# Optimization experiments

Measured on AMD Instinct MI355X. Metric: run time of the kernel, lower is better.

## Reference

```python
import jax, jax.numpy as jnp
import numpy as np

N_LIG, M_POC = 16384, 32768
E_LIG, E_POC, K_CROSS = 163840, 327680, 8
H = 64
L = 4

silu = jax.nn.silu


def _lin(k, fan_in, fan_out):
    k1, k2 = jax.random.split(k)
    s = 1.0 / np.sqrt(fan_in)
    W = jax.random.uniform(k1, (fan_in, fan_out), jnp.float32, -s, s)
    b = jax.random.uniform(k2, (fan_out,), jnp.float32, -s, s)
    return W, b


def setup_inputs() -> dict:
    key = jax.random.key(0)
    ks = jax.random.split(key, 32)
    inp = {
        'lig_x': jax.random.normal(ks[0], (N_LIG, 3), jnp.float32),
        'lig_h': jax.random.normal(ks[1], (N_LIG, 17), jnp.float32),
        'poc_x': jax.random.normal(ks[2], (M_POC, 3), jnp.float32),
        'poc_h': jax.random.normal(ks[3], (M_POC, 29), jnp.float32),
        'lig_edge_index': jax.random.randint(ks[4], (2, E_LIG), 0, N_LIG, jnp.int32),
        'lig_edge_attr': jax.random.normal(ks[5], (E_LIG, 6), jnp.float32),
        'poc_edge_index': jax.random.randint(ks[6], (2, E_POC), 0, M_POC, jnp.int32),
        'poc_edge_attr': jax.random.normal(ks[7], (E_POC, 16), jnp.float32),
        'cross_edge_index': jnp.stack([
            jax.random.randint(ks[8], (N_LIG * K_CROSS,), 0, M_POC, jnp.int32),
            jax.random.randint(ks[9], (N_LIG * K_CROSS,), 0, N_LIG, jnp.int32)]),
        'cross_edge_attr': jax.random.normal(ks[10], (N_LIG * K_CROSS, 16), jnp.float32),
        't': jax.random.uniform(ks[11], (1,), jnp.float32),
    }
    # embeddings
    inp['lig_emb_W'], inp['lig_emb_b'] = _lin(ks[12], 18, H)
    inp['poc_emb_W'], inp['poc_emb_b'] = _lin(ks[13], 29, H)
    inp['lig_ee_W'], inp['lig_ee_b'] = _lin(ks[14], 6, H)
    inp['poc_ee_W'], inp['poc_ee_b'] = _lin(ks[15], 16, H)
    inp['cross_ee_W'], inp['cross_ee_b'] = _lin(ks[16], 16, H)
    # per-layer params stacked along leading L axis
    def stack(kk, fan_in, fan_out):
        Ws, bs = zip(*[_lin(k, fan_in, fan_out) for k in jax.random.split(kk, L)])
        return jnp.stack(Ws), jnp.stack(bs)
    inp['phi_e_W1'], inp['phi_e_b1'] = stack(ks[17], 2 * H + 1 + H, H)
    inp['phi_e_W2'], inp['phi_e_b2'] = stack(ks[18], H, H)
    inp['phi_x_W1'], inp['phi_x_b1'] = stack(ks[19], H, H)
    inp['phi_x_W2'], inp['phi_x_b2'] = stack(ks[20], H, 1)
    inp['phi_h_W1'], inp['phi_h_b1'] = stack(ks[21], 2 * H, H)
    inp['phi_h_W2'], inp['phi_h_b2'] = stack(ks[22], H, H)
    inp['out_W1'], inp['out_b1'] = _lin(ks[23], H, H)
    inp['out_W2'], inp['out_b2'] = _lin(ks[24], H, 1)
    return inp


def _forward(lig_x, lig_h, poc_x, poc_h, lig_edge_attr, poc_edge_attr,
             cross_edge_attr, t,
             lig_emb_W, lig_emb_b, poc_emb_W, poc_emb_b,
             lig_ee_W, lig_ee_b, poc_ee_W, poc_ee_b, cross_ee_W, cross_ee_b,
             phi_e_W1, phi_e_b1, phi_e_W2, phi_e_b2,
             phi_x_W1, phi_x_b1, phi_x_W2, phi_x_b2,
             phi_h_W1, phi_h_b1, phi_h_W2, phi_h_b2,
             out_W1, out_b1, out_W2, out_b2,
             lig_edge_index, poc_edge_index, cross_edge_index):
    n_lig = lig_h.shape[0]
    n_tot = n_lig + poc_h.shape[0]
    t_feat = jnp.broadcast_to(t.reshape(1, 1), (n_lig, 1))
    h_lig = jnp.concatenate([lig_h, t_feat], -1) @ lig_emb_W + lig_emb_b
    h_poc = poc_h @ poc_emb_W + poc_emb_b
    h = jnp.concatenate([h_lig, h_poc], 0)          # [N, H]
    x = jnp.concatenate([lig_x, poc_x], 0)          # [N, 3]
    src = jnp.concatenate([lig_edge_index[0], poc_edge_index[0] + n_lig,
                           cross_edge_index[0] + n_lig])
    dst = jnp.concatenate([lig_edge_index[1], poc_edge_index[1] + n_lig,
                           cross_edge_index[1]])
    eattr = jnp.concatenate([
        lig_edge_attr @ lig_ee_W + lig_ee_b,
        poc_edge_attr @ poc_ee_W + poc_ee_b,
        cross_edge_attr @ cross_ee_W + cross_ee_b], 0)  # [E, H]
    # True = pocket => coords not updated
    update_mask = jnp.concatenate([
        jnp.ones((n_lig, 1), h.dtype), jnp.zeros((n_tot - n_lig, 1), h.dtype)], 0)
    for i in range(phi_e_W1.shape[0]):
        diff = x[src] - x[dst]                                    # [E, 3]
        dist = jnp.sum(diff * diff, -1, keepdims=True) / 100.0    # [E, 1]
        e_in = jnp.concatenate([h[src], h[dst], dist, eattr], -1) # [E, 2H+1+H]
        m = silu(silu(e_in @ phi_e_W1[i] + phi_e_b1[i]) @ phi_e_W2[i] + phi_e_b2[i])
        cw = jnp.tanh(silu(m @ phi_x_W1[i] + phi_x_b1[i]) @ phi_x_W2[i] + phi_x_b2[i])
        coord_agg = jax.ops.segment_sum(diff * cw, dst, num_segments=n_tot) * update_mask
        msg_agg = jax.ops.segment_sum(m, dst, num_segments=n_tot)
        h = h + silu(jnp.concatenate([h, msg_agg], -1) @ phi_h_W1[i] + phi_h_b1[i]) @ phi_h_W2[i] + phi_h_b2[i]
        x = x + coord_agg
    disp = x[:n_lig] - lig_x
    scale = silu(h[:n_lig] @ out_W1 + out_b1) @ out_W2 + out_b2
    return scale * disp


def reference(lig_x, lig_h, poc_x, poc_h, lig_edge_attr, poc_edge_attr,
              cross_edge_attr, t,
              lig_emb_W, lig_emb_b, poc_emb_W, poc_emb_b,
              lig_ee_W, lig_ee_b, poc_ee_W, poc_ee_b, cross_ee_W, cross_ee_b,
              phi_e_W1, phi_e_b1, phi_e_W2, phi_e_b2,
              phi_x_W1, phi_x_b1, phi_x_W2, phi_x_b2,
              phi_h_W1, phi_h_b1, phi_h_W2, phi_h_b2,
              out_W1, out_b1, out_W2, out_b2,
              lig_edge_index, poc_edge_index, cross_edge_index):
    return _forward(lig_x, lig_h, poc_x, poc_h, lig_edge_attr, poc_edge_attr,
                    cross_edge_attr, t,
                    lig_emb_W, lig_emb_b, poc_emb_W, poc_emb_b,
                    lig_ee_W, lig_ee_b, poc_ee_W, poc_ee_b, cross_ee_W, cross_ee_b,
                    phi_e_W1, phi_e_b1, phi_e_W2, phi_e_b2,
                    phi_x_W1, phi_x_b1, phi_x_W2, phi_x_b2,
                    phi_h_W1, phi_h_b1, phi_h_W2, phi_h_b2,
                    out_W1, out_b1, out_W2, out_b2,
                    lig_edge_index, poc_edge_index, cross_edge_index)
```

## Files before the change

kernel.cpp:

```cpp
#include <hip/hip_runtime.h>

#define N_LIG 16384
#define M_POC 32768
#define N_TOT (N_LIG + M_POC)
#define E_LIG 163840
#define E_POC 327680
#define E_CROSS (N_LIG * 8)
#define E_TOT (E_LIG + E_POC + E_CROSS)
#define TE 16

typedef __bf16 bf16_t;
typedef bf16_t bf16x8 __attribute__((ext_vector_type(8)));
typedef bf16_t bf16x4 __attribute__((ext_vector_type(4)));
typedef bf16_t bf16x2 __attribute__((ext_vector_type(2)));
typedef float f32x4 __attribute__((ext_vector_type(4)));

#define S2 72
#define WAVE_BYTES (1792 + 2304 + 256)

__device__ __forceinline__ float silu_f(float v) { return v / (1.0f + __expf(-v)); }

__device__ __forceinline__ float tanh_f(float v) {
    float a = fabsf(v);
    float t = __expf(-2.0f * a);
    float r = (1.0f - t) / (1.0f + t);
    return copysignf(r, v);
}

__device__ __forceinline__ void atomic_add_f32(float* p, float v) {
    __hip_atomic_fetch_add(p, v, __ATOMIC_RELAXED, __HIP_MEMORY_SCOPE_AGENT);
}

__device__ __forceinline__ void lds_fence() {
    asm volatile("s_waitcnt lgkmcnt(0)" ::: "memory");
}


__global__ void k_build_edges(const int* __restrict__ lig_ei, const int* __restrict__ poc_ei,
                              const int* __restrict__ cross_ei,
                              int* __restrict__ srcA, int* __restrict__ dstA,
                              int* __restrict__ cnt) {
    int e = blockIdx.x * blockDim.x + threadIdx.x;
    if (e < N_TOT) cnt[e] = 0;
    if (e >= E_TOT) return;
    int s, d;
    if (e < E_LIG) {
        s = lig_ei[e];
        d = lig_ei[E_LIG + e];
    } else if (e < E_LIG + E_POC) {
        int i = e - E_LIG;
        s = poc_ei[i] + N_LIG;
        d = poc_ei[E_POC + i] + N_LIG;
    } else {
        int i = e - E_LIG - E_POC;
        s = cross_ei[i] + N_LIG;
        d = cross_ei[E_CROSS + i];
    }
    srcA[e] = s;
    dstA[e] = d;
}

__global__ void k_hist(const int* __restrict__ dstA, int* __restrict__ cnt) {
    int e = blockIdx.x * blockDim.x + threadIdx.x;
    if (e < E_TOT) atomicAdd(&cnt[dstA[e]], 1);
}

__global__ __launch_bounds__(1024) void k_scan(const int* __restrict__ cnt,
                                               int* __restrict__ rowptr,
                                               int* __restrict__ cursor) {
    __shared__ int sums[1024];
    int tid = threadIdx.x;
    int local[48];
    int s = 0;
    for (int i = 0; i < 48; ++i) { local[i] = s; s += cnt[tid * 48 + i]; }
    sums[tid] = s;
    __syncthreads();
    for (int off = 1; off < 1024; off <<= 1) {
        int v = (tid >= off) ? sums[tid - off] : 0;
        __syncthreads();
        sums[tid] += v;
        __syncthreads();
    }
    int base = (tid == 0) ? 0 : sums[tid - 1];
    for (int i = 0; i < 48; ++i) {
        int v = base + local[i];
        int idx = tid * 48 + i;
        rowptr[idx] = v;
        cursor[idx] = v;
    }
    if (tid == 1023) rowptr[N_TOT] = sums[1023];
}

__global__ void k_scatter(const int* __restrict__ dstA, int* __restrict__ cursor,
                          int* __restrict__ sortedPos) {
    int e = blockIdx.x * blockDim.x + threadIdx.x;
    if (e < E_TOT) sortedPos[e] = atomicAdd(&cursor[dstA[e]], 1);
}

#define PK_G1   (12 * 5 * 4 * 64)
#define PK_G23  (4 * 4 * 4 * 64)
#define PK_WP   (4 * 48 * 256)
#define PK_BEFF (12 * 64)
#define PK_TOT  (PK_G1 + PK_G23 + PK_WP + PK_BEFF)

__global__ void k_pack_all(const float* __restrict__ phi_e_W1, const float* __restrict__ phi_e_b1,
                           const float* __restrict__ lig_ee_W, const float* __restrict__ lig_ee_b,
                           const float* __restrict__ poc_ee_W, const float* __restrict__ poc_ee_b,
                           const float* __restrict__ cross_ee_W, const float* __restrict__ cross_ee_b,
                           const float* __restrict__ phi_e_W2, const float* __restrict__ phi_x_W1,
                           const float* __restrict__ phi_h_W1, const float* __restrict__ phi_h_W2,
                           bf16_t* __restrict__ Bg1, bf16_t* __restrict__ Bg23,
                           float* __restrict__ Wp, float* __restrict__ beff) {
    int tid = blockIdx.x * blockDim.x + threadIdx.x;
    if (tid < PK_G1) {
        int lt = tid / 1280;
        int rem = tid - lt * 1280;
        int c = rem >> 8;
        int nt = (rem >> 6) & 3;
        int lane = rem & 63;
        int l = lt / 3, t = lt % 3;
        const float* W1l = phi_e_W1 + l * 193 * 64;
        const float* We; int K;
        if (t == 0) { We = lig_ee_W; K = 6; }
        else if (t == 1) { We = poc_ee_W; K = 16; }
        else { We = cross_ee_W; K = 16; }
        int col = nt * 16 + (lane & 15);
        int k0 = c * 32 + (lane >> 4) * 8;
        #pragma unroll
        for (int j = 0; j < 8; ++j) {
            int row = k0 + j;
            float v = 0.0f;
            if (row < 128) v = W1l[row * 64 + col];
            else if (row < 144) {
                int kk = row - 128;
                if (kk < K) {
                    float a = 0.0f;
                    for (int q = 0; q < 64; ++q) a = fmaf(We[kk * 64 + q], W1l[(129 + q) * 64 + col], a);
                    v = a;
                }
            } else if (row == 144) {
                v = W1l[128 * 64 + col];
            }
            Bg1[(size_t)tid * 8 + j] = (bf16_t)v;
        }
    } else if (tid < PK_G1 + PK_G23) {
        int u = tid - PK_G1;
        int lane = u & 63;
        int nt = (u >> 6) & 3;
        int c = (u >> 8) & 3;
        int l = u >> 10;
        const float* W = (c < 2) ? (phi_e_W2 + l * 4096) : (phi_x_W1 + l * 4096);
        int kb = (c & 1) * 32;
        int col = nt * 16 + (lane & 15);
        int k0 = kb + (lane >> 4) * 8;
        #pragma unroll
        for (int j = 0; j < 8; ++j)
            Bg23[(size_t)u * 8 + j] = (bf16_t)W[(k0 + j) * 64 + col];
    } else if (tid < PK_G1 + PK_G23 + PK_WP) {
        int idx = tid - PK_G1 - PK_G23;
        int l = idx / (48 * 256);
        int rem = idx - l * (48 * 256);
        int c = rem / 256;
        int q = rem - c * 256;
        int j = q >> 2;
        int kk = q & 3;
        const float* W; int Ksrc; int k4;
        if (c < 32) { W = phi_h_W1 + l * 128 * 64; Ksrc = 128; k4 = c; }
        else        { W = phi_h_W2 + l * 64 * 64;  Ksrc = 64;  k4 = c - 32; }
        int k = k4 * 4 + kk;
        Wp[idx] = (k < Ksrc) ? W[k * 64 + j] : 0.0f;
    } else if (tid < PK_TOT) {
        int u = tid - PK_G1 - PK_G23 - PK_WP;
        int j = u & 63;
        int lt = u >> 6;
        int l = lt / 3, t = lt % 3;
        const float* W1l = phi_e_W1 + l * 193 * 64;
        const float* Be = (t == 0) ? lig_ee_b : ((t == 1) ? poc_ee_b : cross_ee_b);
        float v = phi_e_b1[l * 64 + j];
        for (int q = 0; q < 64; ++q) v = fmaf(Be[q], W1l[(129 + q) * 64 + j], v);
        beff[u] = v;
    }
}

__global__ void k_embed(const float* __restrict__ lig_x, const float* __restrict__ lig_h,
                        const float* __restrict__ poc_x, const float* __restrict__ poc_h,
                        const float* __restrict__ t,
                        const float* __restrict__ ligW, const float* __restrict__ ligB,
                        const float* __restrict__ pocW, const float* __restrict__ pocB,
                        float* __restrict__ h, bf16_t* __restrict__ hB, float* __restrict__ x4) {
    int gid = blockIdx.x * blockDim.x + threadIdx.x;
    int n = gid >> 6;
    int lane = gid & 63;
    if (n >= N_TOT) return;
    float a;
    if (n < N_LIG) {
        a = ligB[lane];
        #pragma unroll
        for (int k = 0; k < 17; ++k) a = fmaf(lig_h[n * 17 + k], ligW[k * 64 + lane], a);
        a = fmaf(t[0], ligW[17 * 64 + lane], a);
        if (lane < 4) x4[n * 4 + lane] = (lane < 3) ? lig_x[n * 3 + lane] : 0.0f;
    } else {
        int p = n - N_LIG;
        a = pocB[lane];
        #pragma unroll
        for (int k = 0; k < 29; ++k) a = fmaf(poc_h[p * 29 + k], pocW[k * 64 + lane], a);
        if (lane < 4) x4[n * 4 + lane] = (lane < 3) ? poc_x[p * 3 + lane] : 0.0f;
    }
    h[n * 64 + lane] = a;
    hB[n * 64 + lane] = (bf16_t)a;
}

__global__ __launch_bounds__(256, 6) void k_edge_mfma(
    const bf16_t* __restrict__ hB, const float* __restrict__ x4,
    const int* __restrict__ srcA, const int* __restrict__ dstA,
    const int* __restrict__ sortedPos,
    const float* __restrict__ lig_attr, const float* __restrict__ poc_attr,
    const float* __restrict__ cross_attr,
    const bf16_t* __restrict__ Bg1L,
    const float* __restrict__ beffL,
    const bf16_t* __restrict__ Bg23L,
    const float* __restrict__ b2, const float* __restrict__ bx1,
    const float* __restrict__ Wx2, const float* __restrict__ bx2,
    bf16_t* __restrict__ mBuf, float* __restrict__ coord_agg) {
    __shared__ __align__(16) char lds[4 * WAVE_BYTES];
    const int lane = threadIdx.x & 63;
    const int wave = threadIdx.x >> 6;
    bf16_t* exL = (bf16_t*)(lds + wave * WAVE_BYTES);
    bf16_t* mA  = (bf16_t*)(lds + wave * WAVE_BYTES + 1792);
    float*  dfL = (float*)(lds + wave * WAVE_BYTES + 1792 + 2304);
    const int base = (blockIdx.x * 4 + wave) * TE;

    int tt; const float* attrBase; int astride;
    if (base < E_LIG) { tt = 0; attrBase = lig_attr + (size_t)base * 6; astride = 6; }
    else if (base < E_LIG + E_POC) { tt = 1; attrBase = poc_attr + (size_t)(base - E_LIG) * 16; astride = 16; }
    else { tt = 2; attrBase = cross_attr + (size_t)(base - E_LIG - E_POC) * 16; astride = 16; }

    const int e16 = base + (lane & 15);
    const int sv = srcA[e16];
    const int dv = dstA[e16];
    const int sp = sortedPos[e16];

    const int mcol = lane & 15;
    const int kgrp = lane >> 4;
    const int mrow0 = kgrp * 4;

    bf16x8 af0 = *(const bf16x8*)(hB + (size_t)sv * 64 + kgrp * 8);
    bf16x8 af1 = *(const bf16x8*)(hB + (size_t)sv * 64 + 32 + kgrp * 8);
    bf16x8 af2 = *(const bf16x8*)(hB + (size_t)dv * 64 + kgrp * 8);
    bf16x8 af3 = *(const bf16x8*)(hB + (size_t)dv * 64 + 32 + kgrp * 8);

    {
        bf16x8 z = {(bf16_t)0.f, (bf16_t)0.f, (bf16_t)0.f, (bf16_t)0.f,
                    (bf16_t)0.f, (bf16_t)0.f, (bf16_t)0.f, (bf16_t)0.f};
        *(bf16x8*)(exL + (lane >> 2) * 56 + (lane & 3) * 8) = z;
    }
    lds_fence();
    if (lane < 16) {
        float4 xs = *(const float4*)(x4 + (size_t)sv * 4);
        float4 xd = *(const float4*)(x4 + (size_t)dv * 4);
        float d0 = xs.x - xd.x;
        float d1 = xs.y - xd.y;
        float d2 = xs.z - xd.z;
        float dist = (d0 * d0 + d1 * d1 + d2 * d2) * 0.01f;
        exL[lane * 56 + 16] = (bf16_t)dist;
        *(float4*)(dfL + lane * 4) = (float4){d0, d1, d2, dist};
        const float* attr = attrBase + lane * astride;
        if (tt == 0) {
            float2 a0 = *(const float2*)(attr);
            float2 a1 = *(const float2*)(attr + 2);
            float2 a2 = *(const float2*)(attr + 4);
            bf16x8 w0 = {(bf16_t)a0.x, (bf16_t)a0.y, (bf16_t)a1.x, (bf16_t)a1.y,
                         (bf16_t)a2.x, (bf16_t)a2.y, (bf16_t)0.f, (bf16_t)0.f};
            *(bf16x8*)(exL + lane * 56) = w0;
        } else {
            float4 a0 = *(const float4*)(attr);
            float4 a1 = *(const float4*)(attr + 4);
            float4 a2 = *(const float4*)(attr + 8);
            float4 a3 = *(const float4*)(attr + 12);
            bf16x8 w0 = {(bf16_t)a0.x, (bf16_t)a0.y, (bf16_t)a0.z, (bf16_t)a0.w,
                         (bf16_t)a1.x, (bf16_t)a1.y, (bf16_t)a1.z, (bf16_t)a1.w};
            bf16x8 w1 = {(bf16_t)a2.x, (bf16_t)a2.y, (bf16_t)a2.z, (bf16_t)a2.w,
                         (bf16_t)a3.x, (bf16_t)a3.y, (bf16_t)a3.z, (bf16_t)a3.w};
            *(bf16x8*)(exL + lane * 56) = w0;
            *(bf16x8*)(exL + lane * 56 + 8) = w1;
        }
    }
    lds_fence();

    const bf16_t* Bg1 = Bg1L + (size_t)tt * 5 * 4 * 512;
    const float* beff = beffL + tt * 64;
    f32x4 acc1[4];
    #pragma unroll
    for (int nt = 0; nt < 4; ++nt) {
        float bv = beff[nt * 16 + mcol];
        acc1[nt] = (f32x4){bv, bv, bv, bv};
    }
    bf16x8 af4 = *(const bf16x8*)(exL + mcol * 56 + kgrp * 8);
    bf16x8 afs[5] = {af0, af1, af2, af3, af4};
    #pragma unroll
    for (int c = 0; c < 5; ++c) {
        #pragma unroll
        for (int nt = 0; nt < 4; ++nt) {
            bf16x8 bfr = *(const bf16x8*)(Bg1 + ((size_t)(c * 4 + nt) * 64 + lane) * 8);
            acc1[nt] = __builtin_amdgcn_mfma_f32_16x16x32_bf16(afs[c], bfr, acc1[nt], 0, 0, 0);
        }
    }
    #pragma unroll
    for (int nt = 0; nt < 4; ++nt)
        #pragma unroll
        for (int g = 0; g < 4; ++g)
            mA[(mrow0 + g) * S2 + nt * 16 + mcol] = (bf16_t)silu_f(acc1[nt][g]);
    lds_fence();

    f32x4 acc2[4];
    #pragma unroll
    for (int nt = 0; nt < 4; ++nt) {
        float bv = b2[nt * 16 + mcol];
        acc2[nt] = (f32x4){bv, bv, bv, bv};
    }
    const bf16_t* aBase2 = mA + mcol * S2 + kgrp * 8;
    #pragma unroll
    for (int c = 0; c < 2; ++c) {
        bf16x8 af = *(const bf16x8*)(aBase2 + c * 32);
        #pragma unroll
        for (int nt = 0; nt < 4; ++nt) {
            bf16x8 bfr = *(const bf16x8*)(Bg23L + ((size_t)(c * 4 + nt) * 64 + lane) * 8);
            acc2[nt] = __builtin_amdgcn_mfma_f32_16x16x32_bf16(af, bfr, acc2[nt], 0, 0, 0);
        }
    }
    lds_fence();
    #pragma unroll
    for (int nt = 0; nt < 4; ++nt)
        #pragma unroll
        for (int g = 0; g < 4; ++g)
            mA[(mrow0 + g) * S2 + nt * 16 + mcol] = (bf16_t)silu_f(acc2[nt][g]);
    lds_fence();

    #pragma unroll
    for (int p = 0; p < 2; ++p) {
        const int r = p * 8 + (lane >> 3);
        const int c8 = (lane & 7) * 8;
        bf16x8 mrow = *(const bf16x8*)(mA + r * S2 + c8);
        const int pos = __shfl(sp, r, 64);
        *(bf16x8*)(mBuf + (size_t)pos * 64 + c8) = mrow;
    }

    f32x4 acc3[4];
    #pragma unroll
    for (int nt = 0; nt < 4; ++nt) {
        float bv = bx1[nt * 16 + mcol];
        acc3[nt] = (f32x4){bv, bv, bv, bv};
    }
    const bf16_t* Bg3 = Bg23L + (size_t)2 * 4 * 512;
    #pragma unroll
    for (int c = 0; c < 2; ++c) {
        bf16x8 af = *(const bf16x8*)(aBase2 + c * 32);
        #pragma unroll
        for (int nt = 0; nt < 4; ++nt) {
            bf16x8 bfr = *(const bf16x8*)(Bg3 + ((size_t)(c * 4 + nt) * 64 + lane) * 8);
            acc3[nt] = __builtin_amdgcn_mfma_f32_16x16x32_bf16(af, bfr, acc3[nt], 0, 0, 0);
        }
    }

    const float bx2v = bx2[0];
    float s[4] = {0.f, 0.f, 0.f, 0.f};
    #pragma unroll
    for (int nt = 0; nt < 4; ++nt) {
        float w = Wx2[nt * 16 + mcol];
        #pragma unroll
        for (int g = 0; g < 4; ++g) s[g] = fmaf(silu_f(acc3[nt][g]), w, s[g]);
    }
    #pragma unroll
    for (int g = 0; g < 4; ++g) {
        float p = s[g];
        #pragma unroll
        for (int off = 1; off < 16; off <<= 1) p += __shfl_xor(p, off, 64);
        const float cw = tanh_f(p + bx2v);
        const int d = __shfl(dv, mrow0 + g, 64);
        if (d < N_LIG && mcol < 3)
            atomic_add_f32(&coord_agg[d * 3 + mcol], dfL[(mrow0 + g) * 4 + mcol] * cw);
    }
}

__global__ __launch_bounds__(256) void k_node(
    float* __restrict__ h, bf16_t* __restrict__ hB, float* __restrict__ x4,
    const bf16_t* __restrict__ mBuf, const int* __restrict__ rowptr,
    float* __restrict__ coord,
    const float* __restrict__ Wh1p, const float* __restrict__ bh1,
    const float* __restrict__ Wh2p, const float* __restrict__ bh2) {
    __shared__ __align__(16) float lds[4][TE * 128];
    const int lane = threadIdx.x & 63;
    const int wave = threadIdx.x >> 6;
    float* inL = lds[wave];
    const int base = (blockIdx.x * 4 + wave) * TE;

    #pragma unroll
    for (int i = 0; i < 4; ++i) {
        int fidx = i * 256 + lane * 4;
        float4 v = *(const float4*)(h + (size_t)base * 64 + fidx);
        *(float4*)(inL + (fidx >> 6) * 128 + (fidx & 63)) = v;
    }

    const int n16 = base + (lane & 15);
    const int rp0 = rowptr[n16];
    const int rp1 = rowptr[n16 + 1];
    const int sub = lane >> 4;
    const int f4 = (lane & 15) * 4;
    for (int r = 0; r < TE; ++r) {
        const int s0 = __shfl(rp0, r, 64);
        const int s1 = __shfl(rp1, r, 64);
        float a0 = 0.f, a1 = 0.f, a2 = 0.f, a3 = 0.f;
        for (int i = s0 + sub; i < s1; i += 4) {
            bf16x4 v = *(const bf16x4*)(mBuf + (size_t)i * 64 + f4);
            a0 += (float)v[0]; a1 += (float)v[1]; a2 += (float)v[2]; a3 += (float)v[3];
        }
        a0 += __shfl_xor(a0, 16, 64); a1 += __shfl_xor(a1, 16, 64);
        a2 += __shfl_xor(a2, 16, 64); a3 += __shfl_xor(a3, 16, 64);
        a0 += __shfl_xor(a0, 32, 64); a1 += __shfl_xor(a1, 32, 64);
        a2 += __shfl_xor(a2, 32, 64); a3 += __shfl_xor(a3, 32, 64);
        if (lane < 16)
            *(float4*)(inL + r * 128 + 64 + f4) = (float4){a0, a1, a2, a3};
    }
    __syncthreads();

    float acc[TE];
    #pragma unroll
    for (int r = 0; r < TE; ++r) acc[r] = bh1[lane];
    for (int c = 0; c < 32; ++c) {
        const float4 w = *(const float4*)(Wh1p + (c * 64 + lane) * 4);
        #pragma unroll
        for (int r = 0; r < TE; ++r) {
            const float4 v = *(const float4*)(inL + r * 128 + c * 4);
            acc[r] = fmaf(v.x, w.x, fmaf(v.y, w.y, fmaf(v.z, w.z, fmaf(v.w, w.w, acc[r]))));
        }
    }
    __syncthreads();
    #pragma unroll
    for (int r = 0; r < TE; ++r) inL[r * 64 + lane] = silu_f(acc[r]);
    __syncthreads();

    float acc2[TE];
    #pragma unroll
    for (int r = 0; r < TE; ++r) acc2[r] = bh2[lane];
    for (int c = 0; c < 16; ++c) {
        const float4 w = *(const float4*)(Wh2p + (c * 64 + lane) * 4);
        #pragma unroll
        for (int r = 0; r < TE; ++r) {
            const float4 v = *(const float4*)(inL + r * 64 + c * 4);
            acc2[r] = fmaf(v.x, w.x, fmaf(v.y, w.y, fmaf(v.z, w.z, fmaf(v.w, w.w, acc2[r]))));
        }
    }
    for (int r = 0; r < TE; ++r) {
        const int n = base + r;
        float hv = h[n * 64 + lane] + acc2[r];
        h[n * 64 + lane] = hv;
        hB[n * 64 + lane] = (bf16_t)hv;
        if (lane < 3) {
            if (n < N_LIG) x4[n * 4 + lane] += coord[n * 3 + lane];
            coord[n * 3 + lane] = 0.0f;
        }
    }
}

__global__ void k_out(const float* __restrict__ h, const float* __restrict__ x4,
                      const float* __restrict__ lig_x,
                      const float* __restrict__ oW1, const float* __restrict__ ob1,
                      const float* __restrict__ oW2, const float* __restrict__ ob2,
                      float* __restrict__ out) {
    int gid = blockIdx.x * blockDim.x + threadIdx.x;
    int n = gid >> 6;
    int lane = gid & 63;
    if (n >= N_LIG) return;
    float hv = h[n * 64 + lane];
    float a = ob1[lane];
    #pragma unroll
    for (int k = 0; k < 64; ++k) a = fmaf(__shfl(hv, k, 64), oW1[k * 64 + lane], a);
    float p = silu_f(a) * oW2[lane];
    #pragma unroll
    for (int off = 32; off > 0; off >>= 1) p += __shfl_xor(p, off, 64);
    float scale = p + ob2[0];
    if (lane < 3) out[n * 3 + lane] = scale * (x4[n * 4 + lane] - lig_x[n * 3 + lane]);
}

extern "C" void kernel_launch(void* const* d_in, const int* in_sizes, int n_in,
                              void* d_out, int out_size, void* d_ws, size_t ws_size,
                              hipStream_t stream) {
    const float* lig_x      = (const float*)d_in[0];
    const float* lig_h      = (const float*)d_in[1];
    const float* poc_x      = (const float*)d_in[2];
    const float* poc_h      = (const float*)d_in[3];
    const int*   lig_ei     = (const int*)d_in[4];
    const float* lig_attr   = (const float*)d_in[5];
    const int*   poc_ei     = (const int*)d_in[6];
    const float* poc_attr   = (const float*)d_in[7];
    const int*   cross_ei   = (const int*)d_in[8];
    const float* cross_attr = (const float*)d_in[9];
    const float* t          = (const float*)d_in[10];
    const float* lig_emb_W  = (const float*)d_in[11];
    const float* lig_emb_b  = (const float*)d_in[12];
    const float* poc_emb_W  = (const float*)d_in[13];
    const float* poc_emb_b  = (const float*)d_in[14];
    const float* lig_ee_W   = (const float*)d_in[15];
    const float* lig_ee_b   = (const float*)d_in[16];
    const float* poc_ee_W   = (const float*)d_in[17];
    const float* poc_ee_b   = (const float*)d_in[18];
    const float* cross_ee_W = (const float*)d_in[19];
    const float* cross_ee_b = (const float*)d_in[20];
    const float* phi_e_W1   = (const float*)d_in[21];
    const float* phi_e_b1   = (const float*)d_in[22];
    const float* phi_e_W2   = (const float*)d_in[23];
    const float* phi_e_b2   = (const float*)d_in[24];
    const float* phi_x_W1   = (const float*)d_in[25];
    const float* phi_x_b1   = (const float*)d_in[26];
    const float* phi_x_W2   = (const float*)d_in[27];
    const float* phi_x_b2   = (const float*)d_in[28];
    const float* phi_h_W1   = (const float*)d_in[29];
    const float* phi_h_b1   = (const float*)d_in[30];
    const float* phi_h_W2   = (const float*)d_in[31];
    const float* phi_h_b2   = (const float*)d_in[32];
    const float* out_W1     = (const float*)d_in[33];
    const float* out_b1     = (const float*)d_in[34];
    const float* out_W2     = (const float*)d_in[35];
    const float* out_b2     = (const float*)d_in[36];

    char* p = (char*)d_ws;
    auto carve = [&](size_t bytes) { char* r = p; p += (bytes + 255) & ~(size_t)255; return r; };
    float*  h      = (float*)carve((size_t)N_TOT * 64 * 4);
    bf16_t* hB     = (bf16_t*)carve((size_t)N_TOT * 64 * 2);
    float*  x4     = (float*)carve((size_t)N_TOT * 4 * 4);
    float*  coord  = (float*)carve((size_t)N_TOT * 3 * 4);
    float*  Wp     = (float*)carve((size_t)4 * 48 * 256 * 4);
    float*  beff   = (float*)carve((size_t)12 * 64 * 4);
    bf16_t* Bg1    = (bf16_t*)carve((size_t)12 * 5 * 4 * 512 * 2);
    bf16_t* Bg23   = (bf16_t*)carve((size_t)4 * 16 * 512 * 2);
    int*    srcA   = (int*)carve((size_t)E_TOT * 4);
    int*    dstA   = (int*)carve((size_t)E_TOT * 4);
    int*    sortedPos = (int*)carve((size_t)E_TOT * 4);
    int*    cnt    = (int*)carve((size_t)N_TOT * 4);
    int*    cursor = (int*)carve((size_t)N_TOT * 4);
    int*    rowptr = (int*)carve((size_t)(N_TOT + 1) * 4);
    bf16_t* mBuf   = (bf16_t*)carve((size_t)E_TOT * 64 * 2);

    k_build_edges<<<E_TOT / 256, 256, 0, stream>>>(lig_ei, poc_ei, cross_ei, srcA, dstA, cnt);
    k_hist<<<E_TOT / 256, 256, 0, stream>>>(dstA, cnt);
    k_scan<<<1, 1024, 0, stream>>>(cnt, rowptr, cursor);
    k_scatter<<<E_TOT / 256, 256, 0, stream>>>(dstA, cursor, sortedPos);
    k_pack_all<<<(PK_TOT + 255) / 256, 256, 0, stream>>>(
        phi_e_W1, phi_e_b1, lig_ee_W, lig_ee_b, poc_ee_W, poc_ee_b, cross_ee_W, cross_ee_b,
        phi_e_W2, phi_x_W1, phi_h_W1, phi_h_W2, Bg1, Bg23, Wp, beff);
    k_embed<<<(N_TOT * 64) / 256, 256, 0, stream>>>(
        lig_x, lig_h, poc_x, poc_h, t, lig_emb_W, lig_emb_b, poc_emb_W, poc_emb_b, h, hB, x4);
    hipMemsetAsync(coord, 0, (size_t)N_TOT * 3 * 4, stream);

    for (int l = 0; l < 4; ++l) {
        k_edge_mfma<<<E_TOT / 64, 256, 0, stream>>>(
            hB, x4, srcA, dstA, sortedPos, lig_attr, poc_attr, cross_attr,
            Bg1 + (size_t)l * 3 * 5 * 4 * 512, beff + (size_t)l * 3 * 64,
            Bg23 + (size_t)l * 16 * 512,
            phi_e_b2 + l * 64, phi_x_b1 + l * 64,
            phi_x_W2 + l * 64, phi_x_b2 + l,
            mBuf, coord);
        k_node<<<N_TOT / 64, 256, 0, stream>>>(
            h, hB, x4, mBuf, rowptr, coord,
            Wp + (size_t)l * 48 * 256, phi_h_b1 + l * 64,
            Wp + (size_t)l * 48 * 256 + 32 * 256, phi_h_b2 + l * 64);
    }

    k_out<<<(N_LIG * 64) / 256, 256, 0, stream>>>(
        h, x4, lig_x, out_W1, out_b1, out_W2, out_b2, (float*)d_out);
}
```

Before: 888.1 us.

## Move node MLP to bf16 MFMA and transpose edge MFMA operand roles

```diff
diff --git a/kernel.cpp b/kernel.cpp
--- a/kernel.cpp
+++ b/kernel.cpp
@@ -15,8 +15,8 @@
 typedef bf16_t bf16x2 __attribute__((ext_vector_type(2)));
 typedef float f32x4 __attribute__((ext_vector_type(4)));
 
-#define S2 72
-#define WAVE_BYTES (1792 + 2304 + 256)
+#define SM 72
+#define WAVE_BYTES (1792 + 2304 + 2304 + 256)
 
 __device__ __forceinline__ float silu_f(float v) { return v / (1.0f + __expf(-v)); }
 
@@ -99,9 +99,9 @@
 
 #define PK_G1   (12 * 5 * 4 * 64)
 #define PK_G23  (4 * 4 * 4 * 64)
-#define PK_WP   (4 * 48 * 256)
+#define PK_WH   (4 * 24 * 64)
 #define PK_BEFF (12 * 64)
-#define PK_TOT  (PK_G1 + PK_G23 + PK_WP + PK_BEFF)
+#define PK_TOT  (PK_G1 + PK_G23 + PK_WH + PK_BEFF)
 
 __global__ void k_pack_all(const float* __restrict__ phi_e_W1, const float* __restrict__ phi_e_b1,
                            const float* __restrict__ lig_ee_W, const float* __restrict__ lig_ee_b,
@@ -110,13 +110,13 @@
                            const float* __restrict__ phi_e_W2, const float* __restrict__ phi_x_W1,
                            const float* __restrict__ phi_h_W1, const float* __restrict__ phi_h_W2,
                            bf16_t* __restrict__ Bg1, bf16_t* __restrict__ Bg23,
-                           float* __restrict__ Wp, float* __restrict__ beff) {
+                           bf16_t* __restrict__ WhP, float* __restrict__ beff) {
     int tid = blockIdx.x * blockDim.x + threadIdx.x;
     if (tid < PK_G1) {
         int lt = tid / 1280;
         int rem = tid - lt * 1280;
         int c = rem >> 8;
-        int nt = (rem >> 6) & 3;
+        int ft = (rem >> 6) & 3;
         int lane = rem & 63;
         int l = lt / 3, t = lt % 3;
         const float* W1l = phi_e_W1 + l * 193 * 64;
@@ -124,7 +124,7 @@
         if (t == 0) { We = lig_ee_W; K = 6; }
         else if (t == 1) { We = poc_ee_W; K = 16; }
         else { We = cross_ee_W; K = 16; }
-        int col = nt * 16 + (lane & 15);
+        int col = ft * 16 + (lane & 15);
         int k0 = c * 32 + (lane >> 4) * 8;
         #pragma unroll
         for (int j = 0; j < 8; ++j) {
@@ -146,31 +146,31 @@
     } else if (tid < PK_G1 + PK_G23) {
         int u = tid - PK_G1;
         int lane = u & 63;
-        int nt = (u >> 6) & 3;
+        int ft = (u >> 6) & 3;
         int c = (u >> 8) & 3;
         int l = u >> 10;
         const float* W = (c < 2) ? (phi_e_W2 + l * 4096) : (phi_x_W1 + l * 4096);
         int kb = (c & 1) * 32;
-        int col = nt * 16 + (lane & 15);
+        int col = ft * 16 + (lane & 15);
         int k0 = kb + (lane >> 4) * 8;
         #pragma unroll
         for (int j = 0; j < 8; ++j)
             Bg23[(size_t)u * 8 + j] = (bf16_t)W[(k0 + j) * 64 + col];
-    } else if (tid < PK_G1 + PK_G23 + PK_WP) {
-        int idx = tid - PK_G1 - PK_G23;
-        int l = idx / (48 * 256);
-        int rem = idx - l * (48 * 256);
-        int c = rem / 256;
-        int q = rem - c * 256;
-        int j = q >> 2;
-        int kk = q & 3;
-        const float* W; int Ksrc; int k4;
-        if (c < 32) { W = phi_h_W1 + l * 128 * 64; Ksrc = 128; k4 = c; }
-        else        { W = phi_h_W2 + l * 64 * 64;  Ksrc = 64;  k4 = c - 32; }
-        int k = k4 * 4 + kk;
-        Wp[idx] = (k < Ksrc) ? W[k * 64 + j] : 0.0f;
+    } else if (tid < PK_G1 + PK_G23 + PK_WH) {
+        int u = tid - PK_G1 - PK_G23;
+        int lane = u & 63;
+        int frag = (u >> 6) % 24;
+        int l = (u >> 6) / 24;
+        const float* W; int kc, ft;
+        if (frag < 16) { W = phi_h_W1 + l * 128 * 64; kc = frag >> 2; ft = frag & 3; }
+        else           { W = phi_h_W2 + l * 64 * 64;  kc = (frag - 16) >> 2; ft = (frag - 16) & 3; }
+        int col = ft * 16 + (lane & 15);
+        int k0 = kc * 32 + (lane >> 4) * 8;
+        #pragma unroll
+        for (int j = 0; j < 8; ++j)
+            WhP[(size_t)u * 8 + j] = (bf16_t)W[(k0 + j) * 64 + col];
     } else if (tid < PK_TOT) {
-        int u = tid - PK_G1 - PK_G23 - PK_WP;
+        int u = tid - PK_G1 - PK_G23 - PK_WH;
         int j = u & 63;
         int lt = u >> 6;
         int l = lt / 3, t = lt % 3;
@@ -226,8 +226,9 @@
     const int lane = threadIdx.x & 63;
     const int wave = threadIdx.x >> 6;
     bf16_t* exL = (bf16_t*)(lds + wave * WAVE_BYTES);
-    bf16_t* mA  = (bf16_t*)(lds + wave * WAVE_BYTES + 1792);
-    float*  dfL = (float*)(lds + wave * WAVE_BYTES + 1792 + 2304);
+    bf16_t* mT1 = (bf16_t*)(lds + wave * WAVE_BYTES + 1792);
+    bf16_t* mT2 = (bf16_t*)(lds + wave * WAVE_BYTES + 1792 + 2304);
+    float*  dfL = (float*)(lds + wave * WAVE_BYTES + 1792 + 2304 + 2304);
     const int base = (blockIdx.x * 4 + wave) * TE;
 
     int tt; const float* attrBase; int astride;
@@ -235,19 +236,18 @@
     else if (base < E_LIG + E_POC) { tt = 1; attrBase = poc_attr + (size_t)(base - E_LIG) * 16; astride = 16; }
     else { tt = 2; attrBase = cross_attr + (size_t)(base - E_LIG - E_POC) * 16; astride = 16; }
 
-    const int e16 = base + (lane & 15);
+    const int edge = lane & 15;
+    const int kgrp = lane >> 4;
+    const int mrow0 = kgrp * 4;
+    const int e16 = base + edge;
     const int sv = srcA[e16];
     const int dv = dstA[e16];
     const int sp = sortedPos[e16];
 
-    const int mcol = lane & 15;
-    const int kgrp = lane >> 4;
-    const int mrow0 = kgrp * 4;
-
-    bf16x8 af0 = *(const bf16x8*)(hB + (size_t)sv * 64 + kgrp * 8);
-    bf16x8 af1 = *(const bf16x8*)(hB + (size_t)sv * 64 + 32 + kgrp * 8);
-    bf16x8 af2 = *(const bf16x8*)(hB + (size_t)dv * 64 + kgrp * 8);
-    bf16x8 af3 = *(const bf16x8*)(hB + (size_t)dv * 64 + 32 + kgrp * 8);
+    bf16x8 bf0 = *(const bf16x8*)(hB + (size_t)sv * 64 + kgrp * 8);
+    bf16x8 bf1 = *(const bf16x8*)(hB + (size_t)sv * 64 + 32 + kgrp * 8);
+    bf16x8 bf2 = *(const bf16x8*)(hB + (size_t)dv * 64 + kgrp * 8);
+    bf16x8 bf3 = *(const bf16x8*)(hB + (size_t)dv * 64 + 32 + kgrp * 8);
 
     {
         bf16x8 z = {(bf16_t)0.f, (bf16_t)0.f, (bf16_t)0.f, (bf16_t)0.f,
@@ -291,126 +291,116 @@
     const float* beff = beffL + tt * 64;
     f32x4 acc1[4];
     #pragma unroll
-    for (int nt = 0; nt < 4; ++nt) {
-        float bv = beff[nt * 16 + mcol];
-        acc1[nt] = (f32x4){bv, bv, bv, bv};
-    }
-    bf16x8 af4 = *(const bf16x8*)(exL + mcol * 56 + kgrp * 8);
-    bf16x8 afs[5] = {af0, af1, af2, af3, af4};
+    for (int ft = 0; ft < 4; ++ft) {
+        float4 bv = *(const float4*)(beff + ft * 16 + mrow0);
+        acc1[ft] = (f32x4){bv.x, bv.y, bv.z, bv.w};
+    }
+    bf16x8 bf4 = *(const bf16x8*)(exL + edge * 56 + kgrp * 8);
+    bf16x8 bdat[5] = {bf0, bf1, bf2, bf3, bf4};
     #pragma unroll
     for (int c = 0; c < 5; ++c) {
         #pragma unroll
-        for (int nt = 0; nt < 4; ++nt) {
-            bf16x8 bfr = *(const bf16x8*)(Bg1 + ((size_t)(c * 4 + nt) * 64 + lane) * 8);
-            acc1[nt] = __builtin_amdgcn_mfma_f32_16x16x32_bf16(afs[c], bfr, acc1[nt], 0, 0, 0);
-        }
-    }
-    #pragma unroll
-    for (int nt = 0; nt < 4; ++nt)
-        #pragma unroll
-        for (int g = 0; g < 4; ++g)
-            mA[(mrow0 + g) * S2 + nt * 16 + mcol] = (bf16_t)silu_f(acc1[nt][g]);
+        for (int ft = 0; ft < 4; ++ft) {
+            bf16x8 wfr = *(const bf16x8*)(Bg1 + ((size_t)(c * 4 + ft) * 64 + lane) * 8);
+            acc1[ft] = __builtin_amdgcn_mfma_f32_16x16x32_bf16(wfr, bdat[c], acc1[ft], 0, 0, 0);
+        }
+    }
+    #pragma unroll
+    for (int ft = 0; ft < 4; ++ft) {
+        bf16x4 v = {(bf16_t)silu_f(acc1[ft][0]), (bf16_t)silu_f(acc1[ft][1]),
+                    (bf16_t)silu_f(acc1[ft][2]), (bf16_t)silu_f(acc1[ft][3])};
+        *(bf16x4*)(mT1 + edge * SM + ft * 16 + mrow0) = v;
+    }
     lds_fence();
 
     f32x4 acc2[4];
     #pragma unroll
-    for (int nt = 0; nt < 4; ++nt) {
-        float bv = b2[nt * 16 + mcol];
-        acc2[nt] = (f32x4){bv, bv, bv, bv};
-    }
-    const bf16_t* aBase2 = mA + mcol * S2 + kgrp * 8;
+    for (int ft = 0; ft < 4; ++ft) {
+        float4 bv = *(const float4*)(b2 + ft * 16 + mrow0);
+        acc2[ft] = (f32x4){bv.x, bv.y, bv.z, bv.w};
+    }
+    bf16x8 m1f0 = *(const bf16x8*)(mT1 + edge * SM + kgrp * 8);
+    bf16x8 m1f1 = *(const bf16x8*)(mT1 + edge * SM + 32 + kgrp * 8);
     #pragma unroll
     for (int c = 0; c < 2; ++c) {
-        bf16x8 af = *(const bf16x8*)(aBase2 + c * 32);
-        #pragma unroll
-        for (int nt = 0; nt < 4; ++nt) {
-            bf16x8 bfr = *(const bf16x8*)(Bg23L + ((size_t)(c * 4 + nt) * 64 + lane) * 8);
-            acc2[nt] = __builtin_amdgcn_mfma_f32_16x16x32_bf16(af, bfr, acc2[nt], 0, 0, 0);
-        }
+        bf16x8 df = (c == 0) ? m1f0 : m1f1;
+        #pragma unroll
+        for (int ft = 0; ft < 4; ++ft) {
+            bf16x8 wfr = *(const bf16x8*)(Bg23L + ((size_t)(c * 4 + ft) * 64 + lane) * 8);
+            acc2[ft] = __builtin_amdgcn_mfma_f32_16x16x32_bf16(wfr, df, acc2[ft], 0, 0, 0);
+        }
+    }
+    #pragma unroll
+    for (int ft = 0; ft < 4; ++ft) {
+        bf16x4 v = {(bf16_t)silu_f(acc2[ft][0]), (bf16_t)silu_f(acc2[ft][1]),
+                    (bf16_t)silu_f(acc2[ft][2]), (bf16_t)silu_f(acc2[ft][3])};
+        *(bf16x4*)(mT2 + edge * SM + ft * 16 + mrow0) = v;
+        *(bf16x4*)(mBuf + (size_t)sp * 64 + ft * 16 + mrow0) = v;
     }
     lds_fence();
-    #pragma unroll
-    for (int nt = 0; nt < 4; ++nt)
-        #pragma unroll
-        for (int g = 0; g < 4; ++g)
-            mA[(mrow0 + g) * S2 + nt * 16 + mcol] = (bf16_t)silu_f(acc2[nt][g]);
-    lds_fence();
-
-    #pragma unroll
-    for (int p = 0; p < 2; ++p) {
-        const int r = p * 8 + (lane >> 3);
-        const int c8 = (lane & 7) * 8;
-        bf16x8 mrow = *(const bf16x8*)(mA + r * S2 + c8);
-        const int pos = __shfl(sp, r, 64);
-        *(bf16x8*)(mBuf + (size_t)pos * 64 + c8) = mrow;
-    }
 
     f32x4 acc3[4];
     #pragma unroll
-    for (int nt = 0; nt < 4; ++nt) {
-        float bv = bx1[nt * 16 + mcol];
-        acc3[nt] = (f32x4){bv, bv, bv, bv};
-    }
+    for (int ft = 0; ft < 4; ++ft) {
+        float4 bv = *(const float4*)(bx1 + ft * 16 + mrow0);
+        acc3[ft] = (f32x4){bv.x, bv.y, bv.z, bv.w};
+    }
+    bf16x8 mf0 = *(const bf16x8*)(mT2 + edge * SM + kgrp * 8);
+    bf16x8 mf1 = *(const bf16x8*)(mT2 + edge * SM + 32 + kgrp * 8);
     const bf16_t* Bg3 = Bg23L + (size_t)2 * 4 * 512;
     #pragma unroll
     for (int c = 0; c < 2; ++c) {
-        bf16x8 af = *(const bf16x8*)(aBase2 + c * 32);
-        #pragma unroll
-        for (int nt = 0; nt < 4; ++nt) {
-            bf16x8 bfr = *(const bf16x8*)(Bg3 + ((size_t)(c * 4 + nt) * 64 + lane) * 8);
-            acc3[nt] = __builtin_amdgcn_mfma_f32_16x16x32_bf16(af, bfr, acc3[nt], 0, 0, 0);
-        }
-    }
-
-    const float bx2v = bx2[0];
-    float s[4] = {0.f, 0.f, 0.f, 0.f};
-    #pragma unroll
-    for (int nt = 0; nt < 4; ++nt) {
-        float w = Wx2[nt * 16 + mcol];
-        #pragma unroll
-        for (int g = 0; g < 4; ++g) s[g] = fmaf(silu_f(acc3[nt][g]), w, s[g]);
-    }
-    #pragma unroll
-    for (int g = 0; g < 4; ++g) {
-        float p = s[g];
-        #pragma unroll
-        for (int off = 1; off < 16; off <<= 1) p += __shfl_xor(p, off, 64);
-        const float cw = tanh_f(p + bx2v);
-        const int d = __shfl(dv, mrow0 + g, 64);
-        if (d < N_LIG && mcol < 3)
-            atomic_add_f32(&coord_agg[d * 3 + mcol], dfL[(mrow0 + g) * 4 + mcol] * cw);
-    }
-}
-
+        bf16x8 df = (c == 0) ? mf0 : mf1;
+        #pragma unroll
+        for (int ft = 0; ft < 4; ++ft) {
+            bf16x8 wfr = *(const bf16x8*)(Bg3 + ((size_t)(c * 4 + ft) * 64 + lane) * 8);
+            acc3[ft] = __builtin_amdgcn_mfma_f32_16x16x32_bf16(wfr, df, acc3[ft], 0, 0, 0);
+        }
+    }
+
+    float s = 0.0f;
+    #pragma unroll
+    for (int ft = 0; ft < 4; ++ft) {
+        float4 wv = *(const float4*)(Wx2 + ft * 16 + mrow0);
+        s = fmaf(silu_f(acc3[ft][0]), wv.x, s);
+        s = fmaf(silu_f(acc3[ft][1]), wv.y, s);
+        s = fmaf(silu_f(acc3[ft][2]), wv.z, s);
+        s = fmaf(silu_f(acc3[ft][3]), wv.w, s);
+    }
+    s += __shfl_xor(s, 16, 64);
+    s += __shfl_xor(s, 32, 64);
+    const float cw = tanh_f(s + bx2[0]);
+    if (dv < N_LIG && kgrp < 3)
+        atomic_add_f32(&coord_agg[dv * 3 + kgrp], dfL[edge * 4 + kgrp] * cw);
+}
+
+#define NODE_WAVE_BYTES (2304 + 2304)
 __global__ __launch_bounds__(256) void k_node(
     float* __restrict__ h, bf16_t* __restrict__ hB, float* __restrict__ x4,
     const bf16_t* __restrict__ mBuf, const int* __restrict__ rowptr,
     float* __restrict__ coord,
-    const float* __restrict__ Wh1p, const float* __restrict__ bh1,
-    const float* __restrict__ Wh2p, const float* __restrict__ bh2) {
-    __shared__ __align__(16) float lds[4][TE * 128];
+    const bf16_t* __restrict__ WhL,
+    const float* __restrict__ bh1, const float* __restrict__ bh2) {
+    __shared__ __align__(16) char lds[4 * NODE_WAVE_BYTES];
     const int lane = threadIdx.x & 63;
     const int wave = threadIdx.x >> 6;
-    float* inL = lds[wave];
+    bf16_t* msgT = (bf16_t*)(lds + wave * NODE_WAVE_BYTES);
+    bf16_t* mid  = (bf16_t*)(lds + wave * NODE_WAVE_BYTES + 2304);
     const int base = (blockIdx.x * 4 + wave) * TE;
 
-    #pragma unroll
-    for (int i = 0; i < 4; ++i) {
-        int fidx = i * 256 + lane * 4;
-        float4 v = *(const float4*)(h + (size_t)base * 64 + fidx);
-        *(float4*)(inL + (fidx >> 6) * 128 + (fidx & 63)) = v;
-    }
-
-    const int n16 = base + (lane & 15);
+    const int node = lane & 15;
+    const int kgrp = lane >> 4;
+    const int mrow0 = kgrp * 4;
+    const int n16 = base + node;
+
     const int rp0 = rowptr[n16];
     const int rp1 = rowptr[n16 + 1];
-    const int sub = lane >> 4;
-    const int f4 = (lane & 15) * 4;
+    const int f4 = node * 4;
     for (int r = 0; r < TE; ++r) {
         const int s0 = __shfl(rp0, r, 64);
         const int s1 = __shfl(rp1, r, 64);
         float a0 = 0.f, a1 = 0.f, a2 = 0.f, a3 = 0.f;
-        for (int i = s0 + sub; i < s1; i += 4) {
+        for (int i = s0 + kgrp; i < s1; i += 4) {
             bf16x4 v = *(const bf16x4*)(mBuf + (size_t)i * 64 + f4);
             a0 += (float)v[0]; a1 += (float)v[1]; a2 += (float)v[2]; a3 += (float)v[3];
         }
@@ -418,47 +408,70 @@
         a2 += __shfl_xor(a2, 16, 64); a3 += __shfl_xor(a3, 16, 64);
         a0 += __shfl_xor(a0, 32, 64); a1 += __shfl_xor(a1, 32, 64);
         a2 += __shfl_xor(a2, 32, 64); a3 += __shfl_xor(a3, 32, 64);
-        if (lane < 16)
-            *(float4*)(inL + r * 128 + 64 + f4) = (float4){a0, a1, a2, a3};
-    }
-    __syncthreads();
-
-    float acc[TE];
-    #pragma unroll
-    for (int r = 0; r < TE; ++r) acc[r] = bh1[lane];
-    for (int c = 0; c < 32; ++c) {
-        const float4 w = *(const float4*)(Wh1p + (c * 64 + lane) * 4);
-        #pragma unroll
-        for (int r = 0; r < TE; ++r) {
-            const float4 v = *(const float4*)(inL + r * 128 + c * 4);
-            acc[r] = fmaf(v.x, w.x, fmaf(v.y, w.y, fmaf(v.z, w.z, fmaf(v.w, w.w, acc[r]))));
-        }
-    }
-    __syncthreads();
-    #pragma unroll
-    for (int r = 0; r < TE; ++r) inL[r * 64 + lane] = silu_f(acc[r]);
-    __syncthreads();
-
-    float acc2[TE];
-    #pragma unroll
-    for (int r = 0; r < TE; ++r) acc2[r] = bh2[lane];
-    for (int c = 0; c < 16; ++c) {
-        const float4 w = *(const float4*)(Wh2p + (c * 64 + lane) * 4);
-        #pragma unroll
-        for (int r = 0; r < TE; ++r) {
-            const float4 v = *(const float4*)(inL + r * 64 + c * 4);
-            acc2[r] = fmaf(v.x, w.x, fmaf(v.y, w.y, fmaf(v.z, w.z, fmaf(v.w, w.w, acc2[r]))));
-        }
-    }
-    for (int r = 0; r < TE; ++r) {
-        const int n = base + r;
-        float hv = h[n * 64 + lane] + acc2[r];
-        h[n * 64 + lane] = hv;
-        hB[n * 64 + lane] = (bf16_t)hv;
-        if (lane < 3) {
-            if (n < N_LIG) x4[n * 4 + lane] += coord[n * 3 + lane];
-            coord[n * 3 + lane] = 0.0f;
-        }
+        if (lane < 16) {
+            bf16x4 v = {(bf16_t)a0, (bf16_t)a1, (bf16_t)a2, (bf16_t)a3};
+            *(bf16x4*)(msgT + r * SM + f4) = v;
+        }
+    }
+    lds_fence();
+
+    f32x4 acc[4];
+    #pragma unroll
+    for (int ft = 0; ft < 4; ++ft) {
+        float4 bv = *(const float4*)(bh1 + ft * 16 + mrow0);
+        acc[ft] = (f32x4){bv.x, bv.y, bv.z, bv.w};
+    }
+    bf16x8 d0 = *(const bf16x8*)(hB + (size_t)n16 * 64 + kgrp * 8);
+    bf16x8 d1 = *(const bf16x8*)(hB + (size_t)n16 * 64 + 32 + kgrp * 8);
+    bf16x8 d2 = *(const bf16x8*)(msgT + node * SM + kgrp * 8);
+    bf16x8 d3 = *(const bf16x8*)(msgT + node * SM + 32 + kgrp * 8);
+    bf16x8 bdat[4] = {d0, d1, d2, d3};
+    #pragma unroll
+    for (int c = 0; c < 4; ++c) {
+        #pragma unroll
+        for (int ft = 0; ft < 4; ++ft) {
+            bf16x8 wfr = *(const bf16x8*)(WhL + ((size_t)(c * 4 + ft) * 64 + lane) * 8);
+            acc[ft] = __builtin_amdgcn_mfma_f32_16x16x32_bf16(wfr, bdat[c], acc[ft], 0, 0, 0);
+        }
+    }
+    #pragma unroll
+    for (int ft = 0; ft < 4; ++ft) {
+        bf16x4 v = {(bf16_t)silu_f(acc[ft][0]), (bf16_t)silu_f(acc[ft][1]),
+                    (bf16_t)silu_f(acc[ft][2]), (bf16_t)silu_f(acc[ft][3])};
+        *(bf16x4*)(mid + node * SM + ft * 16 + mrow0) = v;
+    }
+    lds_fence();
+
+    f32x4 acc2[4];
+    #pragma unroll
+    for (int ft = 0; ft < 4; ++ft) {
+        float4 bv = *(const float4*)(bh2 + ft * 16 + mrow0);
+        acc2[ft] = (f32x4){bv.x, bv.y, bv.z, bv.w};
+    }
+    bf16x8 g0 = *(const bf16x8*)(mid + node * SM + kgrp * 8);
+    bf16x8 g1 = *(const bf16x8*)(mid + node * SM + 32 + kgrp * 8);
+    #pragma unroll
+    for (int c = 0; c < 2; ++c) {
+        bf16x8 df = (c == 0) ? g0 : g1;
+        #pragma unroll
+        for (int ft = 0; ft < 4; ++ft) {
+            bf16x8 wfr = *(const bf16x8*)(WhL + ((size_t)(16 + c * 4 + ft) * 64 + lane) * 8);
+            acc2[ft] = __builtin_amdgcn_mfma_f32_16x16x32_bf16(wfr, df, acc2[ft], 0, 0, 0);
+        }
+    }
+
+    #pragma unroll
+    for (int ft = 0; ft < 4; ++ft) {
+        float* hp = h + (size_t)n16 * 64 + ft * 16 + mrow0;
+        float4 hv = *(const float4*)hp;
+        hv.x += acc2[ft][0]; hv.y += acc2[ft][1]; hv.z += acc2[ft][2]; hv.w += acc2[ft][3];
+        *(float4*)hp = hv;
+        bf16x4 hb = {(bf16_t)hv.x, (bf16_t)hv.y, (bf16_t)hv.z, (bf16_t)hv.w};
+        *(bf16x4*)(hB + (size_t)n16 * 64 + ft * 16 + mrow0) = hb;
+    }
+    if (kgrp < 3) {
+        if (n16 < N_LIG) x4[n16 * 4 + kgrp] += coord[n16 * 3 + kgrp];
+        coord[n16 * 3 + kgrp] = 0.0f;
     }
 }
 
@@ -529,7 +542,7 @@
     bf16_t* hB     = (bf16_t*)carve((size_t)N_TOT * 64 * 2);
     float*  x4     = (float*)carve((size_t)N_TOT * 4 * 4);
     float*  coord  = (float*)carve((size_t)N_TOT * 3 * 4);
-    float*  Wp     = (float*)carve((size_t)4 * 48 * 256 * 4);
+    bf16_t* WhP    = (bf16_t*)carve((size_t)4 * 24 * 512 * 2);
     float*  beff   = (float*)carve((size_t)12 * 64 * 4);
     bf16_t* Bg1    = (bf16_t*)carve((size_t)12 * 5 * 4 * 512 * 2);
     bf16_t* Bg23   = (bf16_t*)carve((size_t)4 * 16 * 512 * 2);
@@ -547,7 +560,7 @@
     k_scatter<<<E_TOT / 256, 256, 0, stream>>>(dstA, cursor, sortedPos);
     k_pack_all<<<(PK_TOT + 255) / 256, 256, 0, stream>>>(
         phi_e_W1, phi_e_b1, lig_ee_W, lig_ee_b, poc_ee_W, poc_ee_b, cross_ee_W, cross_ee_b,
-        phi_e_W2, phi_x_W1, phi_h_W1, phi_h_W2, Bg1, Bg23, Wp, beff);
+        phi_e_W2, phi_x_W1, phi_h_W1, phi_h_W2, Bg1, Bg23, WhP, beff);
     k_embed<<<(N_TOT * 64) / 256, 256, 0, stream>>>(
         lig_x, lig_h, poc_x, poc_h, t, lig_emb_W, lig_emb_b, poc_emb_W, poc_emb_b, h, hB, x4);
     hipMemsetAsync(coord, 0, (size_t)N_TOT * 3 * 4, stream);
@@ -562,8 +575,8 @@
             mBuf, coord);
         k_node<<<N_TOT / 64, 256, 0, stream>>>(
             h, hB, x4, mBuf, rowptr, coord,
-            Wp + (size_t)l * 48 * 256, phi_h_b1 + l * 64,
-            Wp + (size_t)l * 48 * 256 + 32 * 256, phi_h_b2 + l * 64);
+            WhP + (size_t)l * 24 * 512,
+            phi_h_b1 + l * 64, phi_h_b2 + l * 64);
     }
 
     k_out<<<(N_LIG * 64) / 256, 256, 0, stream>>>(
```

Result: no change. 877.0 us (-1.2%).
